# Kernel tuning notes

Hardware: AMD Instinct MI355X
Metric: run time of the kernel (lower is better)

## Reference

```python
import jax, jax.numpy as jnp
import numpy as np
from jax import lax

DIM = 256
QK = 256
HEADS = 8
NWIN = 7
TOPK = 4
KS = 5
SCALE = QK ** (-0.5)


def setup_inputs() -> dict:
    key = jax.random.key(0)
    ks = jax.random.split(key, 5)
    N, H, W = 8, 56, 56
    x = jax.random.normal(ks[0], (N, H, W, DIM), jnp.float32)
    W_qkv = jax.random.normal(ks[1], (DIM, QK + QK + DIM), jnp.float32) * 0.02
    b_qkv = jnp.zeros((QK + QK + DIM,), jnp.float32)
    lepe_w = jax.random.normal(ks[2], (DIM, 1, KS, KS), jnp.float32) * 0.05  # OIHW depthwise
    lepe_b = jnp.zeros((DIM,), jnp.float32)
    W_o = jax.random.normal(ks[3], (DIM, DIM), jnp.float32) * 0.02
    b_o = jnp.zeros((DIM,), jnp.float32)
    return {"x": x, "W_qkv": W_qkv, "b_qkv": b_qkv, "lepe_w": lepe_w,
            "lepe_b": lepe_b, "W_o": W_o, "b_o": b_o}


def reference(x, W_qkv, b_qkv, lepe_w, lepe_b, W_o, b_o):
    N, H, Wd, C = x.shape
    j = i = NWIN
    h, w = H // j, Wd // i
    p2, w2 = j * i, h * w
    hd, hdv = QK // HEADS, DIM // HEADS

    # window partition: n (j h) (i w) c -> n (j i) h w c
    xw = x.reshape(N, j, h, i, w, C).transpose(0, 1, 3, 2, 4, 5).reshape(N, p2, h, w, C)

    qkv = xw @ W_qkv + b_qkv                       # [N, p2, h, w, 2*QK+DIM... actually QK+(QK+DIM)]
    q = qkv[..., :QK]                              # [N, p2, h, w, QK]
    kv = qkv[..., QK:]                             # [N, p2, h, w, QK+DIM]

    q_pix = q.reshape(N, p2, w2, QK)
    kv_pix = kv.reshape(N, p2, w2, QK + DIM)       # identity kv_down

    q_win = q.mean(axis=(2, 3))                    # [N, p2, QK]
    k_win = kv[..., :QK].mean(axis=(2, 3))         # [N, p2, QK]

    # LePE: depthwise conv on v, in image layout
    v_img = kv[..., QK:].reshape(N, j, i, h, w, DIM).transpose(0, 5, 1, 3, 2, 4).reshape(N, DIM, H, Wd)
    pad = KS // 2
    lepe = lax.conv_general_dilated(v_img, lepe_w, (1, 1), [(pad, pad), (pad, pad)],
                                    feature_group_count=DIM)
    lepe = lepe + lepe_b[None, :, None, None]
    lepe = lepe.transpose(0, 2, 3, 1)              # [N, H, W, DIM]

    # coarse routing (detached in original when diff_routing=False)
    qd = lax.stop_gradient(q_win)
    kd = lax.stop_gradient(k_win)
    logit = jnp.einsum('npc,nqc->npq', qd * SCALE, kd)   # [N, p2, p2]
    _, r_idx = lax.top_k(logit, TOPK)              # [N, p2, TOPK]

    # gather top-k windows of kv (mul_weight='none')
    nidx = jnp.arange(N)[:, None, None]
    kv_sel = kv_pix[nidx, r_idx]                   # [N, p2, TOPK, w2, QK+DIM]
    k_sel = kv_sel[..., :QK].reshape(N, p2, TOPK * w2, HEADS, hd).transpose(0, 1, 3, 2, 4)
    v_sel = kv_sel[..., QK:].reshape(N, p2, TOPK * w2, HEADS, hdv).transpose(0, 1, 3, 2, 4)
    qh = q_pix.reshape(N, p2, w2, HEADS, hd).transpose(0, 1, 3, 2, 4)

    attn = jax.nn.softmax(jnp.einsum('npmwc,npmkc->npmwk', qh * SCALE, k_sel), axis=-1)
    out = jnp.einsum('npmwk,npmkc->npmwc', attn, v_sel)  # [N, p2, HEADS, w2, hdv]

    # back to image: (n p2) m (h w) c -> n (j h) (i w) (m c)
    out = out.transpose(0, 1, 3, 2, 4).reshape(N, j, i, h, w, DIM)
    out = out.transpose(0, 1, 3, 2, 4, 5).reshape(N, H, Wd, DIM)

    out = out + lepe
    out = out @ W_o + b_o
    return out
```

## Files before the change

kernel.cpp:

```cpp
#include <hip/hip_runtime.h>
#include <hip/hip_bf16.h>
#include <math.h>

#define NBATCH 8
#define HWDIM  56
#define NWIN   7
#define P2     49
#define HEADS  8
#define TOPK   4
#define SCALE  0.0625f
#define NPIX   (NBATCH*HWDIM*HWDIM)

typedef __attribute__((ext_vector_type(8))) short bf16x8;
typedef __attribute__((ext_vector_type(4))) float f32x4;

#define GLOBAL_AS __attribute__((address_space(1)))
#define LDS_AS    __attribute__((address_space(3)))

__device__ __forceinline__ void gload16(const unsigned short* g, unsigned short* l) {
  __builtin_amdgcn_global_load_lds((const GLOBAL_AS unsigned int*)g,
                                   (LDS_AS unsigned int*)l, 16, 0, 0);
}

__device__ __forceinline__ unsigned short f2bf(float f) {
  __hip_bfloat16 h = __float2bfloat16(f);
  return *reinterpret_cast<unsigned short*>(&h);
}
__device__ __forceinline__ float bf2f(unsigned short h) {
  return __uint_as_float(((unsigned)h) << 16);
}

__global__ __launch_bounds__(256) void fused_pre(
    const float* __restrict__ x, const float* __restrict__ W_qkv,
    const float* __restrict__ b_qkv, const float* __restrict__ W_o,
    const float* __restrict__ lepe_w,
    unsigned short* __restrict__ xb, float* __restrict__ q_win,
    float* __restrict__ k_win, unsigned short* __restrict__ Wt_qkv,
    unsigned short* __restrict__ Wt_o, float* __restrict__ b_s,
    float* __restrict__ Wc)
{
  __shared__ float4 red[256];
  __shared__ float xs[256];
  const int bidx = blockIdx.x;
  const int t = threadIdx.x;

  if (bidx < NBATCH * P2) {
    const int n = bidx / P2, p = bidx - n * P2;
    const int y0 = (p / NWIN) * 8, x0 = (p % NWIN) * 8;
    const int c4 = t & 63, pg = t >> 6;
    float4 s = {0.f, 0.f, 0.f, 0.f};
    #pragma unroll
    for (int k = 0; k < 16; ++k) {
      const int pix = pg * 16 + k;
      const int yy = y0 + (pix >> 3), xx = x0 + (pix & 7);
      const size_t off = ((size_t)((n * HWDIM + yy) * HWDIM + xx)) * 256 + c4 * 4;
      float4 v = *(const float4*)&x[off];
      ushort4 o = { f2bf(v.x), f2bf(v.y), f2bf(v.z), f2bf(v.w) };
      *(ushort4*)&xb[off] = o;
      s.x += v.x; s.y += v.y; s.z += v.z; s.w += v.w;
    }
    red[t] = s;
    __syncthreads();
    if (pg == 0) {
      float4 a = red[c4], b = red[64 + c4], c = red[128 + c4], d = red[192 + c4];
      float4 o = { (a.x + b.x + c.x + d.x) * (1.f/64.f),
                   (a.y + b.y + c.y + d.y) * (1.f/64.f),
                   (a.z + b.z + c.z + d.z) * (1.f/64.f),
                   (a.w + b.w + c.w + d.w) * (1.f/64.f) };
      *(float4*)&xs[c4 * 4] = o;
    }
    __syncthreads();
    float aq = 0.f, ak = 0.f;
    for (int cc = 0; cc < 256; ++cc) {
      const float xv = xs[cc];
      aq = fmaf(xv, W_qkv[cc * 768 + t], aq);
      ak = fmaf(xv, W_qkv[cc * 768 + 256 + t], ak);
    }
    q_win[(size_t)bidx * 256 + t] = aq + b_qkv[t];
    k_win[(size_t)bidx * 256 + t] = ak + b_qkv[256 + t];
  } else {
    const int idx = (bidx - NBATCH * P2) * 256 + t;
    if (idx < 768 * 256) {
      const int nn = idx >> 8, cc = idx & 255;
      float v = W_qkv[cc * 768 + nn];
      if (nn < 256) v *= SCALE;
      Wt_qkv[idx] = f2bf(v);
    } else if (idx < 768 * 256 + 256 * 256) {
      const int j = idx - 768 * 256;
      const int nn = j >> 8, cc = j & 255;
      Wt_o[j] = f2bf(W_o[cc * 256 + nn]);
    } else if (idx < 768 * 256 + 256 * 256 + 768) {
      const int j = idx - (768 * 256 + 256 * 256);
      b_s[j] = b_qkv[j] * (j < 256 ? SCALE : 1.f);
    } else if (idx < 768 * 256 + 256 * 256 + 768 + 25 * 256) {
      const int j = idx - (768 * 256 + 256 * 256 + 768);
      const int tap = j >> 8, cc = j & 255;
      Wc[j] = lepe_w[cc * 25 + tap];
    }
  }
}

__global__ __launch_bounds__(256) void routing_topk(
    const float* __restrict__ q_win, const float* __restrict__ k_win,
    int* __restrict__ r_idx)
{
  __shared__ float qs[256];
  __shared__ float logit[64];
  const int bidx = blockIdx.x;
  const int n = bidx / P2;
  const int t = threadIdx.x;
  qs[t] = q_win[(size_t)bidx * 256 + t];
  __syncthreads();
  const int qq = t >> 2, qt = t & 3;
  if (qq < P2) {
    const float* kb = k_win + ((size_t)(n * P2 + qq)) * 256 + qt * 64;
    float a = 0.f;
    #pragma unroll 8
    for (int i = 0; i < 64; ++i) a = fmaf(qs[qt * 64 + i], kb[i], a);
    a += __shfl_xor(a, 1);
    a += __shfl_xor(a, 2);
    if (qt == 0) logit[qq] = a;
  }
  __syncthreads();
  if (t == 0) {
    float bv0 = -3e38f, bv1 = -3e38f, bv2 = -3e38f, bv3 = -3e38f;
    int bi0 = 0, bi1 = 0, bi2 = 0, bi3 = 0;
    for (int q2 = 0; q2 < P2; ++q2) {
      const float v = logit[q2];
      if (v > bv0) { bv3=bv2; bi3=bi2; bv2=bv1; bi2=bi1; bv1=bv0; bi1=bi0; bv0=v; bi0=q2; }
      else if (v > bv1) { bv3=bv2; bi3=bi2; bv2=bv1; bi2=bi1; bv1=v; bi1=q2; }
      else if (v > bv2) { bv3=bv2; bi3=bi2; bv2=v; bi2=q2; }
      else if (v > bv3) { bv3=v; bi3=q2; }
    }
    int* rp = r_idx + (size_t)bidx * TOPK;
    rp[0] = bi0; rp[1] = bi1; rp[2] = bi2; rp[3] = bi3;
  }
}

template<int MODE>
__global__ __launch_bounds__(512) void gemm_mfma(
    const unsigned short* __restrict__ A,
    const unsigned short* __restrict__ Bt,
    const float* __restrict__ bias,
    unsigned short* __restrict__ C0, unsigned short* __restrict__ C1,
    unsigned short* __restrict__ C2, float* __restrict__ Cf)
{
  __shared__ char smem[49152];
  unsigned short* Asm = (unsigned short*)smem;
  unsigned short* Bsm = (unsigned short*)(smem + 16384);
  float* Cs = (float*)smem;

  const int t = threadIdx.x;
  const int w = t >> 6, l = t & 63;
  const int wr = w >> 2, wc = w & 3;
  const int lr = l & 15, lg = l >> 4;
  const int bm = blockIdx.x, bn = blockIdx.y;
  const int row0 = bm * 128, col0 = bn * 256;

  const f32x4 fzero = {0.f, 0.f, 0.f, 0.f};
  f32x4 acc[4][4];
  #pragma unroll
  for (int m = 0; m < 4; ++m)
    #pragma unroll
    for (int n = 0; n < 4; ++n) acc[m][n] = fzero;

  const int srow  = t >> 3;
  const int skoff = ((t & 7) ^ (srow & 7)) * 8;

  for (int step = 0; step < 4; ++step) {
    const int k0 = step * 64;
    #pragma unroll
    for (int i = 0; i < 2; ++i)
      gload16(&A [(size_t)(row0 + i*64 + srow) * 256 + k0 + skoff],
              Asm + i*4096 + t*8);
    #pragma unroll
    for (int i = 0; i < 4; ++i)
      gload16(&Bt[(size_t)(col0 + i*64 + srow) * 256 + k0 + skoff],
              Bsm + i*4096 + t*8);
    __syncthreads();
    __builtin_amdgcn_s_setprio(1);
    #pragma unroll
    for (int kk = 0; kk < 2; ++kk) {
      bf16x8 af[4], bb[4];
      #pragma unroll
      for (int m = 0; m < 4; ++m)
        af[m] = *(const bf16x8*)&Asm[(wr*64 + m*16 + lr) * 64 + ((kk*4 + lg) ^ (lr & 7)) * 8];
      #pragma unroll
      for (int n = 0; n < 4; ++n)
        bb[n] = *(const bf16x8*)&Bsm[(wc*64 + n*16 + lr) * 64 + ((kk*4 + lg) ^ (lr & 7)) * 8];
      #pragma unroll
      for (int m = 0; m < 4; ++m)
        #pragma unroll
        for (int n = 0; n < 4; ++n)
          acc[m][n] = __builtin_amdgcn_mfma_f32_16x16x32_bf16(af[m], bb[n], acc[m][n], 0, 0, 0);
    }
    __builtin_amdgcn_s_setprio(0);
    __syncthreads();
  }

  float bcol[4];
  #pragma unroll
  for (int n = 0; n < 4; ++n) bcol[n] = bias[col0 + wc*64 + n*16 + lr];

  #pragma unroll
  for (int hf = 0; hf < 4; ++hf) {
    if (hf) __syncthreads();
    if (wr == (hf >> 1)) {
      const int mbase = (hf & 1) * 2;
      #pragma unroll
      for (int mm = 0; mm < 2; ++mm)
        #pragma unroll
        for (int n = 0; n < 4; ++n)
          #pragma unroll
          for (int r = 0; r < 4; ++r) {
            const int lrow = mm*16 + lg*4 + r;
            const int col  = wc*64 + n*16 + lr;
            const int csw  = col ^ ((lrow & 7) << 2);
            Cs[lrow * 256 + csw] = acc[mbase + mm][n][r] + bcol[n];
          }
    }
    __syncthreads();
    #pragma unroll
    for (int it = 0; it < 4; ++it) {
      const int d = (it * 512 + t) * 4;
      const int lrow = d >> 8;
      const int colL = (d & 255) ^ ((lrow & 7) << 2);
      f32x4 v = *(const f32x4*)&Cs[d];
      const size_t grow = (size_t)(row0 + hf*32 + lrow);
      if (MODE == 0) {
        unsigned short* Cp = (bn == 0) ? C0 : (bn == 1) ? C1 : C2;
        ushort4 o = { f2bf(v[0]), f2bf(v[1]), f2bf(v[2]), f2bf(v[3]) };
        *(ushort4*)&Cp[grow * 256 + colL] = o;
      } else {
        float4 o = { v[0], v[1], v[2], v[3] };
        *(float4*)&Cf[grow * 256 + colL] = o;
      }
    }
  }
}

#define PSTR 272

__global__ __launch_bounds__(256) void attn_mfma(
    const unsigned short* __restrict__ q_bf,
    const unsigned short* __restrict__ k_bf,
    const unsigned short* __restrict__ v_bf,
    const int* __restrict__ r_idx,
    const float* __restrict__ Wc,
    const float* __restrict__ lepe_b,
    unsigned short* __restrict__ o_bf)
{
  __shared__ char smem[52480];
  unsigned short* Ksm = (unsigned short*)smem;
  unsigned short* Qsm = (unsigned short*)(smem + 16384);
  unsigned short* Psm = (unsigned short*)smem;
  unsigned short* Vsm = (unsigned short*)(smem + 34816);
  float*          Osm = (float*)(smem + 34816);
  float*          Ls  = (float*)(smem + 52224);

  const int b = blockIdx.x;
  const int h = b & 7;
  const int np = b >> 3;
  const int n = np / P2, p = np - n * P2;
  const int t = threadIdx.x;
  const int w = t >> 6, l = t & 63;
  const int lr = l & 15, lg = l >> 4;

  const int4 rv = *(const int4*)&r_idx[np * 4];

  {
    const int pix = t >> 2, ch = t & 3;
    #pragma unroll
    for (int i = 0; i < 4; ++i) {
      const int wv = (&rv.x)[i];
      const int ky = (wv / NWIN) * 8 + (pix >> 3);
      const int kx = (wv % NWIN) * 8 + (pix & 7);
      const size_t goff = ((size_t)((n * HWDIM + ky) * HWDIM + kx)) * 256 + h * 32;
      gload16(&k_bf[goff + ch * 8], Ksm + i * 2048 + t * 8);
    }
    const int qy = (p / NWIN) * 8 + (pix >> 3);
    const int qx = (p % NWIN) * 8 + (pix & 7);
    gload16(&q_bf[((size_t)((n * HWDIM + qy) * HWDIM + qx)) * 256 + h * 32 + ch * 8],
            Qsm + t * 8);
  }
  {
    const int s = t >> 6, pix = t & 63;
    const int wv = (&rv.x)[s];
    const int ky = (wv / NWIN) * 8 + (pix >> 3);
    const int kx = (wv % NWIN) * 8 + (pix & 7);
    const size_t goff = ((size_t)((n * HWDIM + ky) * HWDIM + kx)) * 256 + h * 32;
    #pragma unroll
    for (int j = 0; j < 4; ++j) {
      bf16x8 vv = *(const bf16x8*)&v_bf[goff + j * 8];
      #pragma unroll
      for (int e = 0; e < 8; ++e)
        Vsm[(j * 8 + e) * PSTR + t] = (unsigned short)vv[e];
    }
  }
  __syncthreads();

  f32x4 sf[16];
  {
    const f32x4 fzero = {0.f, 0.f, 0.f, 0.f};
    bf16x8 aq = *(const bf16x8*)&Qsm[(w * 16 + lr) * 32 + lg * 8];
    __builtin_amdgcn_s_setprio(1);
    #pragma unroll
    for (int f = 0; f < 16; ++f) {
      bf16x8 bk = *(const bf16x8*)&Ksm[(f * 16 + lr) * 32 + lg * 8];
      sf[f] = __builtin_amdgcn_mfma_f32_16x16x32_bf16(bk, aq, fzero, 0, 0, 0);
    }
    __builtin_amdgcn_s_setprio(0);
  }

  {
    float mx = sf[0][0];
    #pragma unroll
    for (int f = 0; f < 16; ++f)
      #pragma unroll
      for (int r = 0; r < 4; ++r) mx = fmaxf(mx, sf[f][r]);
    mx = fmaxf(mx, __shfl_xor(mx, 16));
    mx = fmaxf(mx, __shfl_xor(mx, 32));
    float sum = 0.f;
    #pragma unroll
    for (int f = 0; f < 16; ++f)
      #pragma unroll
      for (int r = 0; r < 4; ++r) {
        float e = __expf(sf[f][r] - mx);
        sf[f][r] = e; sum += e;
      }
    sum += __shfl_xor(sum, 16);
    sum += __shfl_xor(sum, 32);
    if (lg == 0) Ls[w * 16 + lr] = 1.f / sum;
  }
  __syncthreads();

  #pragma unroll
  for (int f = 0; f < 16; ++f) {
    ushort4 pk = { f2bf(sf[f][0]), f2bf(sf[f][1]), f2bf(sf[f][2]), f2bf(sf[f][3]) };
    *(ushort4*)&Psm[(w * 16 + lr) * PSTR + f * 16 + lg * 4] = pk;
  }

  f32x4 oacc[2];
  oacc[0] = (f32x4){0.f, 0.f, 0.f, 0.f};
  oacc[1] = (f32x4){0.f, 0.f, 0.f, 0.f};
  __builtin_amdgcn_s_setprio(1);
  #pragma unroll
  for (int ks = 0; ks < 8; ++ks) {
    bf16x8 ap = *(const bf16x8*)&Psm[(w * 16 + lr) * PSTR + ks * 32 + lg * 8];
    #pragma unroll
    for (int nn = 0; nn < 2; ++nn) {
      bf16x8 bv = *(const bf16x8*)&Vsm[(nn * 16 + lr) * PSTR + ks * 32 + lg * 8];
      oacc[nn] = __builtin_amdgcn_mfma_f32_16x16x32_bf16(ap, bv, oacc[nn], 0, 0, 0);
    }
  }
  __builtin_amdgcn_s_setprio(0);

  float inv4[4];
  #pragma unroll
  for (int r = 0; r < 4; ++r) inv4[r] = Ls[w * 16 + lg * 4 + r];

  __syncthreads();
  #pragma unroll
  for (int nn = 0; nn < 2; ++nn)
    #pragma unroll
    for (int r = 0; r < 4; ++r)
      Osm[(w * 16 + lg * 4 + r) * 36 + nn * 16 + lr] = oacc[nn][r] * inv4[r];
  __syncthreads();

  {
    const int q = t >> 2, dq = (t & 3) * 8;
    const int qy = (p / NWIN) * 8 + (q >> 3);
    const int qx = (p % NWIN) * 8 + (q & 7);
    const int c0 = h * 32 + dq;

    float acc[8];
    {
      float4 b0 = *(const float4*)&lepe_b[c0];
      float4 b1 = *(const float4*)&lepe_b[c0 + 4];
      acc[0]=b0.x; acc[1]=b0.y; acc[2]=b0.z; acc[3]=b0.w;
      acc[4]=b1.x; acc[5]=b1.y; acc[6]=b1.z; acc[7]=b1.w;
    }
    #pragma unroll
    for (int ky = 0; ky < 5; ++ky) {
      const int sy = qy + ky - 2;
      if (sy < 0 || sy >= HWDIM) continue;
      #pragma unroll
      for (int kx = 0; kx < 5; ++kx) {
        const int sx = qx + kx - 2;
        if (sx < 0 || sx >= HWDIM) continue;
        const bf16x8 vv = *(const bf16x8*)&v_bf[((size_t)((n * HWDIM + sy) * HWDIM + sx)) * 256 + c0];
        const float* wp = &Wc[(ky * 5 + kx) * 256 + c0];
        float4 w0 = *(const float4*)wp;
        float4 w1 = *(const float4*)(wp + 4);
        acc[0] = fmaf(w0.x, bf2f((unsigned short)vv[0]), acc[0]);
        acc[1] = fmaf(w0.y, bf2f((unsigned short)vv[1]), acc[1]);
        acc[2] = fmaf(w0.z, bf2f((unsigned short)vv[2]), acc[2]);
        acc[3] = fmaf(w0.w, bf2f((unsigned short)vv[3]), acc[3]);
        acc[4] = fmaf(w1.x, bf2f((unsigned short)vv[4]), acc[4]);
        acc[5] = fmaf(w1.y, bf2f((unsigned short)vv[5]), acc[5]);
        acc[6] = fmaf(w1.z, bf2f((unsigned short)vv[6]), acc[6]);
        acc[7] = fmaf(w1.w, bf2f((unsigned short)vv[7]), acc[7]);
      }
    }
    float vo[8];
    #pragma unroll
    for (int e = 0; e < 8; ++e) vo[e] = Osm[q * 36 + dq + e] + acc[e];
    ushort4 o0 = { f2bf(vo[0]), f2bf(vo[1]), f2bf(vo[2]), f2bf(vo[3]) };
    ushort4 o1 = { f2bf(vo[4]), f2bf(vo[5]), f2bf(vo[6]), f2bf(vo[7]) };
    unsigned short* op = &o_bf[((size_t)((n * HWDIM + qy) * HWDIM + qx)) * 256 + c0];
    *(ushort4*)op = o0;
    *(ushort4*)&op[4] = o1;
  }
}

extern "C" void kernel_launch(void* const* d_in, const int* in_sizes, int n_in,
                              void* d_out, int out_size, void* d_ws, size_t ws_size,
                              hipStream_t stream)
{
  const float* x      = (const float*)d_in[0];
  const float* W_qkv  = (const float*)d_in[1];
  const float* b_qkv  = (const float*)d_in[2];
  const float* lepe_w = (const float*)d_in[3];
  const float* lepe_b = (const float*)d_in[4];
  const float* W_o    = (const float*)d_in[5];
  const float* b_o    = (const float*)d_in[6];
  float* out = (float*)d_out;

  char* ws = (char*)d_ws;
  const size_t IMG = (size_t)NPIX * 256;
  unsigned short* x_bf    = (unsigned short*)(ws);
  unsigned short* q_bf    = (unsigned short*)(ws + 2*IMG);
  unsigned short* k_bf    = (unsigned short*)(ws + 4*IMG);
  unsigned short* v_bf    = (unsigned short*)(ws + 6*IMG);
  unsigned short* attn_bf = (unsigned short*)(ws + 8*IMG);
  unsigned short* Wt_qkv  = (unsigned short*)(ws + 10*IMG);
  unsigned short* Wt_o    = (unsigned short*)(ws + 10*IMG + 393216);
  float*          b_s     = (float*)         (ws + 10*IMG + 393216 + 131072);
  float*          q_win   = (float*)         (ws + 10*IMG + 393216 + 131072 + 4096);
  float*          k_win   = q_win + (size_t)NBATCH * P2 * 256;
  int*            ridx    = (int*)(k_win + (size_t)NBATCH * P2 * 256);
  float*          Wc      = (float*)(ridx + (size_t)NBATCH * P2 * TOPK);

  fused_pre<<<NBATCH * P2 + 1052, 256, 0, stream>>>(
      x, W_qkv, b_qkv, W_o, lepe_w, x_bf, q_win, k_win, Wt_qkv, Wt_o, b_s, Wc);
  routing_topk<<<NBATCH * P2, 256, 0, stream>>>(q_win, k_win, ridx);
  gemm_mfma<0><<<dim3(196, 3), 512, 0, stream>>>(x_bf, Wt_qkv, b_s,
                                                 q_bf, k_bf, v_bf, nullptr);
  attn_mfma<<<NBATCH * P2 * HEADS, 256, 0, stream>>>(q_bf, k_bf, v_bf, ridx,
                                                     Wc, lepe_b, attn_bf);
  gemm_mfma<1><<<dim3(196, 1), 512, 0, stream>>>(attn_bf, Wt_o, b_o,
                                                 nullptr, nullptr, nullptr, out);
}
```

Measured before the change: 213.6 us.

## Stage LePE halo tile and weights in LDS, swizzle P/V layouts

Preloads the 12x12 halo of V for the window, together with the depthwise conv weights and bias, into registers early and stores them to LDS. The 5x5 LePE conv then reads from shared memory instead of issuing 25 scattered global loads per thread. It also replaces the padded PSTR layout for P and V with XOR-swizzled 256-wide rows, which shrinks LDS use and is meant to avoid bank conflicts. The cost is more registers held across the attention phase (vreg, hreg, wreg), which could lower occupancy.

```diff
diff --git a/kernel.cpp b/kernel.cpp
--- a/kernel.cpp
+++ b/kernel.cpp
@@ -239,8 +239,6 @@
   }
 }
 
-#define PSTR 272
-
 __global__ __launch_bounds__(256) void attn_mfma(
     const unsigned short* __restrict__ q_bf,
     const unsigned short* __restrict__ k_bf,
@@ -250,13 +248,16 @@
     const float* __restrict__ lepe_b,
     unsigned short* __restrict__ o_bf)
 {
-  __shared__ char smem[52480];
+  __shared__ char smem[49408];
   unsigned short* Ksm = (unsigned short*)smem;
   unsigned short* Qsm = (unsigned short*)(smem + 16384);
   unsigned short* Psm = (unsigned short*)smem;
-  unsigned short* Vsm = (unsigned short*)(smem + 34816);
-  float*          Osm = (float*)(smem + 34816);
-  float*          Ls  = (float*)(smem + 52224);
+  unsigned short* Vsm = (unsigned short*)(smem + 32768);
+  float*          Osm = (float*)(smem + 32768);
+  unsigned short* Hsm = (unsigned short*)smem;
+  float*          Wsm = (float*)(smem + 9216);
+  float*          Lbs = (float*)(smem + 12416);
+  float*          Ls  = (float*)(smem + 49152);
 
   const int b = blockIdx.x;
   const int h = b & 7;
@@ -265,6 +266,7 @@
   const int t = threadIdx.x;
   const int w = t >> 6, l = t & 63;
   const int lr = l & 15, lg = l >> 4;
+  const int y0 = (p / NWIN) * 8, x0 = (p % NWIN) * 8;
 
   const int4 rv = *(const int4*)&r_idx[np * 4];
 
@@ -278,11 +280,12 @@
       const size_t goff = ((size_t)((n * HWDIM + ky) * HWDIM + kx)) * 256 + h * 32;
       gload16(&k_bf[goff + ch * 8], Ksm + i * 2048 + t * 8);
     }
-    const int qy = (p / NWIN) * 8 + (pix >> 3);
-    const int qx = (p % NWIN) * 8 + (pix & 7);
+    const int qy = y0 + (pix >> 3), qx = x0 + (pix & 7);
     gload16(&q_bf[((size_t)((n * HWDIM + qy) * HWDIM + qx)) * 256 + h * 32 + ch * 8],
             Qsm + t * 8);
   }
+
+  bf16x8 vreg[4];
   {
     const int s = t >> 6, pix = t & 63;
     const int wv = (&rv.x)[s];
@@ -290,12 +293,39 @@
     const int kx = (wv % NWIN) * 8 + (pix & 7);
     const size_t goff = ((size_t)((n * HWDIM + ky) * HWDIM + kx)) * 256 + h * 32;
     #pragma unroll
-    for (int j = 0; j < 4; ++j) {
-      bf16x8 vv = *(const bf16x8*)&v_bf[goff + j * 8];
-      #pragma unroll
-      for (int e = 0; e < 8; ++e)
-        Vsm[(j * 8 + e) * PSTR + t] = (unsigned short)vv[e];
-    }
+    for (int j = 0; j < 4; ++j)
+      vreg[j] = *(const bf16x8*)&v_bf[goff + j * 8];
+  }
+  bf16x8 hreg[3];
+  {
+    const bf16x8 hz = {0,0,0,0,0,0,0,0};
+    #pragma unroll
+    for (int i = 0; i < 3; ++i) {
+      hreg[i] = hz;
+      const int u = t + i * 256;
+      if (u < 576) {
+        const int pu = u >> 2, cu = u & 3;
+        const int hy = pu / 12, hx = pu - hy * 12;
+        const int gy = y0 - 2 + hy, gx = x0 - 2 + hx;
+        if (gy >= 0 && gy < HWDIM && gx >= 0 && gx < HWDIM)
+          hreg[i] = *(const bf16x8*)&v_bf[((size_t)((n * HWDIM + gy) * HWDIM + gx)) * 256 + h * 32 + cu * 8];
+      }
+    }
+  }
+  float4 wreg = {0.f, 0.f, 0.f, 0.f};
+  float  breg = 0.f;
+  if (t < 200) wreg = *(const float4*)&Wc[(t >> 3) * 256 + h * 32 + (t & 7) * 4];
+  else if (t < 232) breg = lepe_b[h * 32 + (t - 200)];
+
+  {
+    const int key = t;
+    #pragma unroll
+    for (int j = 0; j < 4; ++j)
+      #pragma unroll
+      for (int e = 0; e < 8; ++e) {
+        const int d = j * 8 + e;
+        Vsm[d * 256 + (((key >> 3) ^ (d & 7)) << 3) + (key & 7)] = (unsigned short)vreg[j][e];
+      }
   }
   __syncthreads();
 
@@ -337,7 +367,8 @@
   #pragma unroll
   for (int f = 0; f < 16; ++f) {
     ushort4 pk = { f2bf(sf[f][0]), f2bf(sf[f][1]), f2bf(sf[f][2]), f2bf(sf[f][3]) };
-    *(ushort4*)&Psm[(w * 16 + lr) * PSTR + f * 16 + lg * 4] = pk;
+    const int chs = ((f * 2 + (lg >> 1)) ^ (lr & 7));
+    *(ushort4*)&Psm[(w * 16 + lr) * 256 + chs * 8 + (lg & 1) * 4] = pk;
   }
 
   f32x4 oacc[2];
@@ -346,10 +377,11 @@
   __builtin_amdgcn_s_setprio(1);
   #pragma unroll
   for (int ks = 0; ks < 8; ++ks) {
-    bf16x8 ap = *(const bf16x8*)&Psm[(w * 16 + lr) * PSTR + ks * 32 + lg * 8];
+    const int cs = (((ks * 4 + lg) ^ (lr & 7))) << 3;
+    bf16x8 ap = *(const bf16x8*)&Psm[(w * 16 + lr) * 256 + cs];
     #pragma unroll
     for (int nn = 0; nn < 2; ++nn) {
-      bf16x8 bv = *(const bf16x8*)&Vsm[(nn * 16 + lr) * PSTR + ks * 32 + lg * 8];
+      bf16x8 bv = *(const bf16x8*)&Vsm[(nn * 16 + lr) * 256 + cs];
       oacc[nn] = __builtin_amdgcn_mfma_f32_16x16x32_bf16(ap, bv, oacc[nn], 0, 0, 0);
     }
   }
@@ -360,51 +392,56 @@
   for (int r = 0; r < 4; ++r) inv4[r] = Ls[w * 16 + lg * 4 + r];
 
   __syncthreads();
+
   #pragma unroll
   for (int nn = 0; nn < 2; ++nn)
     #pragma unroll
     for (int r = 0; r < 4; ++r)
       Osm[(w * 16 + lg * 4 + r) * 36 + nn * 16 + lr] = oacc[nn][r] * inv4[r];
-  __syncthreads();
-
-  {
-    const int q = t >> 2, dq = (t & 3) * 8;
-    const int qy = (p / NWIN) * 8 + (q >> 3);
-    const int qx = (p % NWIN) * 8 + (q & 7);
-    const int c0 = h * 32 + dq;
-
-    float acc[8];
+  #pragma unroll
+  for (int i = 0; i < 3; ++i) {
+    const int u = t + i * 256;
+    if (u < 576)
+      *(bf16x8*)&Hsm[(u >> 2) * 32 + (u & 3) * 8] = hreg[i];
+  }
+  if (t < 200) *(float4*)&Wsm[(t >> 3) * 32 + (t & 7) * 4] = wreg;
+  else if (t < 232) Lbs[t - 200] = breg;
+  __syncthreads();
+
+  {
+    const int q = t >> 2, dq8 = t & 3;
+    const int qy_l = q >> 3, qx_l = q & 7;
+    const int c0 = h * 32 + dq8 * 8;
+
+    float accv[8];
     {
-      float4 b0 = *(const float4*)&lepe_b[c0];
-      float4 b1 = *(const float4*)&lepe_b[c0 + 4];
-      acc[0]=b0.x; acc[1]=b0.y; acc[2]=b0.z; acc[3]=b0.w;
-      acc[4]=b1.x; acc[5]=b1.y; acc[6]=b1.z; acc[7]=b1.w;
-    }
-    #pragma unroll
-    for (int ky = 0; ky < 5; ++ky) {
-      const int sy = qy + ky - 2;
-      if (sy < 0 || sy >= HWDIM) continue;
+      f32x4 b0 = *(const f32x4*)&Lbs[dq8 * 8];
+      f32x4 b1 = *(const f32x4*)&Lbs[dq8 * 8 + 4];
+      accv[0]=b0[0]; accv[1]=b0[1]; accv[2]=b0[2]; accv[3]=b0[3];
+      accv[4]=b1[0]; accv[5]=b1[1]; accv[6]=b1[2]; accv[7]=b1[3];
+    }
+    #pragma unroll
+    for (int ky = 0; ky < 5; ++ky)
       #pragma unroll
       for (int kx = 0; kx < 5; ++kx) {
-        const int sx = qx + kx - 2;
-        if (sx < 0 || sx >= HWDIM) continue;
-        const bf16x8 vv = *(const bf16x8*)&v_bf[((size_t)((n * HWDIM + sy) * HWDIM + sx)) * 256 + c0];
-        const float* wp = &Wc[(ky * 5 + kx) * 256 + c0];
-        float4 w0 = *(const float4*)wp;
-        float4 w1 = *(const float4*)(wp + 4);
-        acc[0] = fmaf(w0.x, bf2f((unsigned short)vv[0]), acc[0]);
-        acc[1] = fmaf(w0.y, bf2f((unsigned short)vv[1]), acc[1]);
-        acc[2] = fmaf(w0.z, bf2f((unsigned short)vv[2]), acc[2]);
-        acc[3] = fmaf(w0.w, bf2f((unsigned short)vv[3]), acc[3]);
-        acc[4] = fmaf(w1.x, bf2f((unsigned short)vv[4]), acc[4]);
-        acc[5] = fmaf(w1.y, bf2f((unsigned short)vv[5]), acc[5]);
-        acc[6] = fmaf(w1.z, bf2f((unsigned short)vv[6]), acc[6]);
-        acc[7] = fmaf(w1.w, bf2f((unsigned short)vv[7]), acc[7]);
+        const int pix = (qy_l + ky) * 12 + (qx_l + kx);
+        const bf16x8 hv = *(const bf16x8*)&Hsm[pix * 32 + dq8 * 8];
+        const f32x4 w0 = *(const f32x4*)&Wsm[(ky * 5 + kx) * 32 + dq8 * 8];
+        const f32x4 w1 = *(const f32x4*)&Wsm[(ky * 5 + kx) * 32 + dq8 * 8 + 4];
+        accv[0] = fmaf(w0[0], bf2f((unsigned short)hv[0]), accv[0]);
+        accv[1] = fmaf(w0[1], bf2f((unsigned short)hv[1]), accv[1]);
+        accv[2] = fmaf(w0[2], bf2f((unsigned short)hv[2]), accv[2]);
+        accv[3] = fmaf(w0[3], bf2f((unsigned short)hv[3]), accv[3]);
+        accv[4] = fmaf(w1[0], bf2f((unsigned short)hv[4]), accv[4]);
+        accv[5] = fmaf(w1[1], bf2f((unsigned short)hv[5]), accv[5]);
+        accv[6] = fmaf(w1[2], bf2f((unsigned short)hv[6]), accv[6]);
+        accv[7] = fmaf(w1[3], bf2f((unsigned short)hv[7]), accv[7]);
       }
-    }
+
+    const int qy = y0 + qy_l, qx = x0 + qx_l;
     float vo[8];
     #pragma unroll
-    for (int e = 0; e < 8; ++e) vo[e] = Osm[q * 36 + dq + e] + acc[e];
+    for (int e = 0; e < 8; ++e) vo[e] = Osm[q * 36 + dq8 * 8 + e] + accv[e];
     ushort4 o0 = { f2bf(vo[0]), f2bf(vo[1]), f2bf(vo[2]), f2bf(vo[3]) };
     ushort4 o1 = { f2bf(vo[4]), f2bf(vo[5]), f2bf(vo[6]), f2bf(vo[7]) };
     unsigned short* op = &o_bf[((size_t)((n * HWDIM + qy) * HWDIM + qx)) * 256 + c0];
```

New measurement: 212.9 us. Within noise of the previous version (-0.3%).
